# Kernel optimization log

Measured on AMD Instinct MI355X. Metric: run time of the kernel, lower is better.

## Reference

```python
import jax, jax.numpy as jnp
import numpy as np


def _min_euclid_block(x, sh):
    # x: [B, C, T], sh: [C, K, S]
    S = sh.shape[-1]
    T = x.shape[2]
    W = T - S + 1  # number of sliding windows
    idx = jnp.arange(W)[:, None] + jnp.arange(S)[None, :]  # [W, S]
    xu = x[:, :, idx]  # [B, C, W, S] sliding windows (unfold)
    # pairwise euclidean distance via the Gram expansion (same math as cdist)
    x2 = jnp.sum(xu * xu, axis=-1)          # [B, C, W]
    s2 = jnp.sum(sh * sh, axis=-1)          # [C, K]
    xs = jnp.einsum('bcws,cks->bcwk', xu, sh)  # [B, C, W, K]
    d2 = x2[..., None] + s2[None, :, None, :] - 2.0 * xs
    d = jnp.sqrt(jnp.maximum(d2, 1e-12))    # [B, C, W, K]
    d = jnp.sum(d, axis=1, keepdims=True)   # sum over channels -> [B, 1, W, K]
    return jnp.min(d, axis=2)               # min over windows -> [B, 1, K]


def setup_inputs() -> dict:
    key = jax.random.key(0)
    k0, k1, k2, k3 = jax.random.split(key, 4)
    B, C, T, K = 32, 3, 2048, 128
    return {
        'x': jax.random.normal(k0, (B, C, T), dtype=jnp.float32),
        'sh16': jax.random.normal(k1, (C, K, 16), dtype=jnp.float32),
        'sh32': jax.random.normal(k2, (C, K, 32), dtype=jnp.float32),
        'sh64': jax.random.normal(k3, (C, K, 64), dtype=jnp.float32),
    }


def reference(x, sh16, sh32, sh64):
    # ShapeletsDistBlocks with dist_measure='euclidean': run each
    # MinEuclideanDistBlock and concatenate along the shapelet axis (dim 2).
    outs = [_min_euclid_block(x, sh) for sh in (sh16, sh32, sh64)]
    return jnp.concatenate(outs, axis=2)  # [B, 1, sum(K)]
```

## Files before the change

### kernel.cpp

```cpp
#include <hip/hip_runtime.h>

typedef __attribute__((ext_vector_type(8)))  __bf16 bf16x8;
typedef __attribute__((ext_vector_type(16))) float  f32x16;

#define DEV __device__ __forceinline__

namespace {

constexpr int BB = 32, CC = 3, TT = 2048, KK = 128, OUTK = 384;
constexpr int TP = 2176;

constexpr size_t OFF_B16 = 0;
constexpr size_t OFF_B32 = 12288;
constexpr size_t OFF_B64 = 36864;
constexpr size_t OFF_S2  = 86016;
constexpr size_t OFF_X2  = 90624;
constexpr size_t OFF_XC  = 2449920;

DEV unsigned short rne(float f) {
  unsigned u = __float_as_uint(f);
  u += 0x7FFFu + ((u >> 16) & 1u);
  return (unsigned short)(u >> 16);
}
DEV float rnef(float f) {
  unsigned u = __float_as_uint(f);
  u += 0x7FFFu + ((u >> 16) & 1u);
  return __uint_as_float(u & 0xFFFF0000u);
}
DEV uint4 pack8(const unsigned short* h) {
  uint4 d;
  d.x = (unsigned)h[0] | ((unsigned)h[1] << 16);
  d.y = (unsigned)h[2] | ((unsigned)h[3] << 16);
  d.z = (unsigned)h[4] | ((unsigned)h[5] << 16);
  d.w = (unsigned)h[6] | ((unsigned)h[7] << 16);
  return d;
}
DEV float f4get(const float4 v, int j) {
  switch (j) { case 0: return v.x; case 1: return v.y; case 2: return v.z; default: return v.w; }
}

constexpr int N_OUT = BB * OUTK;
constexpr int N_BF  = 5376;
constexpr int N_S2  = 1152;
constexpr int N_XC  = BB * CC * 8 * (TP/8);
constexpr int N_X2  = BB * CC * TT;
constexpr int N_TOT = N_OUT + N_BF + N_S2 + N_XC + N_X2;

__global__ __launch_bounds__(256) void precompute(
    const float* __restrict__ x, const float* __restrict__ sh16,
    const float* __restrict__ sh32, const float* __restrict__ sh64,
    unsigned char* __restrict__ ws, unsigned* __restrict__ outu)
{
  int i = blockIdx.x * 256 + threadIdx.x;
  if (i >= N_TOT) return;
  if (i < N_OUT) { outu[i] = 0x7f800000u; return; }
  i -= N_OUT;

  if (i < N_BF) {
    int S, it; const float* sh; size_t boff;
    if (i < 768)       { S = 16; it = i;        sh = sh16; boff = OFF_B16; }
    else if (i < 2304) { S = 32; it = i - 768;  sh = sh32; boff = OFF_B32; }
    else               { S = 64; it = i - 2304; sh = sh64; boff = OFF_B64; }
    const int CHS = S / 8, KST = S / 16;
    int c = it / (KK * CHS); int r = it - c * KK * CHS;
    int n = r / CHS;         int k0 = (r - n * CHS) * 8;
    const float* src = sh + ((size_t)(c * KK + n)) * S + k0;
    unsigned short h[8];
    #pragma unroll
    for (int j = 0; j < 8; ++j) h[j] = rne(src[j]);
    ((uint4*)(ws + boff))[((c * 4 + (n >> 5)) * KST + (k0 >> 4)) * 64 + ((k0 >> 3) & 1) * 32 + (n & 31)] = pack8(h);
    return;
  }
  i -= N_BF;

  if (i < N_S2) {
    int Sidx = i / 384; int r = i - Sidx * 384; int c = r >> 7; int k = r & 127;
    int S = 16 << Sidx;
    const float* sh = (Sidx == 0) ? sh16 : ((Sidx == 1) ? sh32 : sh64);
    const float* sp = sh + ((size_t)(c * KK + k)) * S;
    float acc = 0.f;
    #pragma unroll 4
    for (int s = 0; s < S; ++s) { float v = rnef(sp[s]); acc = fmaf(v, v, acc); }
    ((float*)(ws + OFF_S2))[(Sidx * CC + c) * KK + k] = acc;
    return;
  }
  i -= N_S2;

  if (i < N_XC) {
    const int per = TP / 8;
    int c8 = i / per; int q8 = i - c8 * per;
    int p  = c8 & 7;  int bc = c8 >> 3;
    const float* xb = x + (size_t)bc * TT;
    int m0 = q8 * 8;
    unsigned short h[8];
    #pragma unroll
    for (int j = 0; j < 8; ++j) {
      int mi = m0 + j + p;
      float v = (mi < TT) ? xb[mi] : 0.f;
      h[j] = rne(v);
    }
    ((uint4*)(ws + OFF_XC + (size_t)c8 * TP * 2))[q8] = pack8(h);
    return;
  }
  i -= N_XC;

  {
    int w = i & (TT - 1); int bc = i >> 11;
    const float* xb = x + (size_t)bc * TT;
    float acc = 0.f, a16, a32, a64;
    #pragma unroll 4
    for (int s = 0; s < 16; ++s) { int mi = w + s; float v = (mi < TT) ? rnef(xb[mi]) : 0.f; acc = fmaf(v, v, acc); }
    a16 = acc;
    #pragma unroll 4
    for (int s = 16; s < 32; ++s) { int mi = w + s; float v = (mi < TT) ? rnef(xb[mi]) : 0.f; acc = fmaf(v, v, acc); }
    a32 = acc;
    #pragma unroll 4
    for (int s = 32; s < 64; ++s) { int mi = w + s; float v = (mi < TT) ? rnef(xb[mi]) : 0.f; acc = fmaf(v, v, acc); }
    a64 = acc;
    float* x2 = (float*)(ws + OFF_X2);
    x2[(size_t)(0 * BB * CC + bc) * TT + w] = a16;
    x2[(size_t)(1 * BB * CC + bc) * TT + w] = a32;
    x2[(size_t)(2 * BB * CC + bc) * TT + w] = a64;
  }
}

DEV void epi(const f32x16 a, const float* __restrict__ x2c, float s2c, int lhi, f32x16& dsum) {
  #pragma unroll
  for (int g = 0; g < 4; ++g) {
    const float4 xq = *(const float4*)(x2c + 4 * lhi + 8 * g);
    #pragma unroll
    for (int j = 0; j < 4; ++j) {
      const int r2 = g * 4 + j;
      dsum[r2] += __builtin_amdgcn_sqrtf(fmaxf(fmaf(-2.f, a[r2], f4get(xq, j) + s2c), 1e-12f));
    }
  }
}

template<int S, int KST, int OUTOFF, size_t BOFF, int SIDX>
DEV void run(const unsigned char* __restrict__ ws, unsigned* __restrict__ outu,
             int r, float* __restrict__ x2l, float* __restrict__ s2l)
{
  const int b = r >> 4, wg = r & 15;
  const int tid = (int)threadIdx.x;
  const int lane = tid & 63, wsub = tid >> 6;
  const int l31 = lane & 31, lhi = lane >> 5, p = l31 & 7;
  const int w0 = wg * 128 + wsub * 32;

  const unsigned short* XCb = (const unsigned short*)(ws + OFF_XC);
  uint4 A[CC][KST];
  #pragma unroll
  for (int c = 0; c < CC; ++c) {
    const unsigned short* xA = XCb + ((size_t)((b * CC + c) * 8) + p) * TP
                             + (w0 + 8 * (l31 >> 3) + 8 * lhi);
    #pragma unroll
    for (int kk = 0; kk < KST; ++kk) A[c][kk] = *(const uint4*)(xA + 16 * kk);
  }

  const float* x2g = (const float*)(ws + OFF_X2) + (size_t)(SIDX * BB * CC + b * CC) * TT + wg * 128;
  const float* s2g = (const float*)(ws + OFF_S2) + SIDX * CC * KK;
  #pragma unroll
  for (int i0 = 0; i0 < 2; ++i0) {
    int i = i0 * 256 + tid;
    if (i < 384) {
      int c = i >> 7, q = i & 127;
      x2l[i] = x2g[(size_t)c * TT + q];
      s2l[i] = s2g[c * KK + q];
    }
  }
  __syncthreads();

  const uint4* Bg = (const uint4*)(ws + BOFF) + lane;
  constexpr int W = TT - S + 1;

  #pragma unroll
  for (int kq = 0; kq < 4; ++kq) {
    f32x16 dsum{};
    #pragma unroll
    for (int c = 0; c < CC; ++c) {
      uint4 Bf[KST];
      #pragma unroll
      for (int kk = 0; kk < KST; ++kk)
        Bf[kk] = Bg[(size_t)(((c * 4 + kq) * KST + kk)) * 64];
      f32x16 acc{};
      #pragma unroll
      for (int kk = 0; kk < KST; ++kk)
        acc = __builtin_amdgcn_mfma_f32_32x32x16_bf16(
            __builtin_bit_cast(bf16x8, A[c][kk]), __builtin_bit_cast(bf16x8, Bf[kk]), acc, 0, 0, 0);
      const float s2c = s2l[c * 128 + kq * 32 + l31];
      epi(acc, x2l + c * 128 + wsub * 32, s2c, lhi, dsum);
    }
    float m = __builtin_inff();
    if (w0 + 31 < W) {
      #pragma unroll
      for (int r2 = 0; r2 < 16; ++r2) m = fminf(m, dsum[r2]);
    } else {
      #pragma unroll
      for (int r2 = 0; r2 < 16; ++r2) {
        const int ro = (r2 & 3) + 8 * (r2 >> 2) + 4 * lhi;
        if (w0 + ro < W) m = fminf(m, dsum[r2]);
      }
    }
    m = fminf(m, __shfl_xor(m, 32));
    if (lane < 32)
      atomicMin(outu + (b * OUTK + OUTOFF + kq * 32 + l31), __float_as_uint(m));
  }
}

__global__ __launch_bounds__(256, 3) void shapelets_main(
    const unsigned char* __restrict__ ws, unsigned* __restrict__ outu)
{
  __shared__ __attribute__((aligned(16))) float x2l[384];
  __shared__ __attribute__((aligned(16))) float s2l[384];
  const int j = (int)blockIdx.x;
  if (j < 512)       run<64, 4, 256, OFF_B64, 2>(ws, outu, j,        x2l, s2l);
  else if (j < 1024) run<32, 2, 128, OFF_B32, 1>(ws, outu, j - 512,  x2l, s2l);
  else               run<16, 1,   0, OFF_B16, 0>(ws, outu, j - 1024, x2l, s2l);
}

}

extern "C" void kernel_launch(void* const* d_in, const int* in_sizes, int n_in,
                              void* d_out, int out_size, void* d_ws, size_t ws_size,
                              hipStream_t stream) {
  const float* x    = (const float*)d_in[0];
  const float* sh16 = (const float*)d_in[1];
  const float* sh32 = (const float*)d_in[2];
  const float* sh64 = (const float*)d_in[3];
  unsigned* outu = (unsigned*)d_out;
  unsigned char* ws = (unsigned char*)d_ws;

  precompute<<<(N_TOT + 255) / 256, 256, 0, stream>>>(x, sh16, sh32, sh64, ws, outu);
  shapelets_main<<<1536, 256, 0, stream>>>(ws, outu);
}
```

Measured before the change: 39.72 us.

## Stage shapelet B fragments through double-buffered LDS with cooperative prefetch

Each block previously had all four waves load the same shapelet B fragments from global memory. The block now loads them cooperatively into a double-buffered LDS staging area, prefetching the next kq chunk into registers while the current one is computed, with a barrier per chunk. The atomicMin writes are also deferred to the end of the block. This cuts redundant global/L2 traffic, but it adds about 24KB of LDS per block, four barriers, and staging registers, which may lower occupancy.

New measurement: 42.69 us. 7.5% more time.

```diff
diff --git a/kernel.cpp b/kernel.cpp
--- a/kernel.cpp
+++ b/kernel.cpp
@@ -136,10 +136,37 @@
   }
 }
 
+template<int KST>
+DEV void stageLoad(const uint4* __restrict__ Bg0, int kq, int tid, uint4 (&st)[3]) {
+  constexpr int TOT = CC * KST * 64;
+  constexpr int NJ  = (TOT + 255) / 256;
+  #pragma unroll
+  for (int j = 0; j < NJ; ++j) {
+    int i = j * 256 + tid;
+    if ((TOT % 256 == 0) || i < TOT) {
+      int slot = i & 63, m = i >> 6;
+      int c = m / KST, kk = m - c * KST;
+      st[j] = Bg0[(size_t)(((c * 4 + kq) * KST + kk)) * 64 + slot];
+    }
+  }
+}
+template<int KST>
+DEV void stageWrite(uint4* __restrict__ lbuf, int tid, const uint4 (&st)[3]) {
+  constexpr int TOT = CC * KST * 64;
+  constexpr int NJ  = (TOT + 255) / 256;
+  #pragma unroll
+  for (int j = 0; j < NJ; ++j) {
+    int i = j * 256 + tid;
+    if ((TOT % 256 == 0) || i < TOT) lbuf[i] = st[j];
+  }
+}
+
 template<int S, int KST, int OUTOFF, size_t BOFF, int SIDX>
 DEV void run(const unsigned char* __restrict__ ws, unsigned* __restrict__ outu,
-             int r, float* __restrict__ x2l, float* __restrict__ s2l)
+             int r, float* __restrict__ x2l, float* __restrict__ s2l,
+             uint4* __restrict__ bbuf)
 {
+  constexpr int CHUNK = CC * KST * 64;
   const int b = r >> 4, wg = r & 15;
   const int tid = (int)threadIdx.x;
   const int lane = tid & 63, wsub = tid >> 6;
@@ -155,6 +182,10 @@
     #pragma unroll
     for (int kk = 0; kk < KST; ++kk) A[c][kk] = *(const uint4*)(xA + 16 * kk);
   }
+
+  const uint4* Bg0 = (const uint4*)(ws + BOFF);
+  uint4 st[3];
+  stageLoad<KST>(Bg0, 0, tid, st);
 
   const float* x2g = (const float*)(ws + OFF_X2) + (size_t)(SIDX * BB * CC + b * CC) * TT + wg * 128;
   const float* s2g = (const float*)(ws + OFF_S2) + SIDX * CC * KK;
@@ -167,20 +198,23 @@
       s2l[i] = s2g[c * KK + q];
     }
   }
+  stageWrite<KST>(bbuf, tid, st);
   __syncthreads();
 
-  const uint4* Bg = (const uint4*)(ws + BOFF) + lane;
   constexpr int W = TT - S + 1;
+  float mq[4];
 
   #pragma unroll
   for (int kq = 0; kq < 4; ++kq) {
+    if (kq < 3) stageLoad<KST>(Bg0, kq + 1, tid, st);
+    const uint4* lb = bbuf + (kq & 1) * CHUNK;
     f32x16 dsum{};
     #pragma unroll
     for (int c = 0; c < CC; ++c) {
       uint4 Bf[KST];
       #pragma unroll
       for (int kk = 0; kk < KST; ++kk)
-        Bf[kk] = Bg[(size_t)(((c * 4 + kq) * KST + kk)) * 64];
+        Bf[kk] = lb[(c * KST + kk) * 64 + lane];
       f32x16 acc{};
       #pragma unroll
       for (int kk = 0; kk < KST; ++kk)
@@ -200,9 +234,17 @@
         if (w0 + ro < W) m = fminf(m, dsum[r2]);
       }
     }
-    m = fminf(m, __shfl_xor(m, 32));
-    if (lane < 32)
-      atomicMin(outu + (b * OUTK + OUTOFF + kq * 32 + l31), __float_as_uint(m));
+    mq[kq] = fminf(m, __shfl_xor(m, 32));
+    if (kq < 3) {
+      stageWrite<KST>(bbuf + ((kq & 1) ^ 1) * CHUNK, tid, st);
+      __syncthreads();
+    }
+  }
+
+  if (lane < 32) {
+    #pragma unroll
+    for (int kq = 0; kq < 4; ++kq)
+      atomicMin(outu + (b * OUTK + OUTOFF + kq * 32 + l31), __float_as_uint(mq[kq]));
   }
 }
 
@@ -211,10 +253,11 @@
 {
   __shared__ __attribute__((aligned(16))) float x2l[384];
   __shared__ __attribute__((aligned(16))) float s2l[384];
+  __shared__ __attribute__((aligned(16))) uint4 bbuf[2 * CC * 4 * 64];
   const int j = (int)blockIdx.x;
-  if (j < 512)       run<64, 4, 256, OFF_B64, 2>(ws, outu, j,        x2l, s2l);
-  else if (j < 1024) run<32, 2, 128, OFF_B32, 1>(ws, outu, j - 512,  x2l, s2l);
-  else               run<16, 1,   0, OFF_B16, 0>(ws, outu, j - 1024, x2l, s2l);
+  if (j < 512)       run<64, 4, 256, OFF_B64, 2>(ws, outu, j,        x2l, s2l, bbuf);
+  else if (j < 1024) run<32, 2, 128, OFF_B32, 1>(ws, outu, j - 512,  x2l, s2l, bbuf);
+  else               run<16, 1,   0, OFF_B16, 0>(ws, outu, j - 1024, x2l, s2l, bbuf);
 }
 
 }
```

## Use single-wave blocks and read x2/s2 from global instead of LDS

Applied to the files above, without the earlier changes.

The main kernel now runs one 64-thread wavefront per block (6144 blocks) instead of four wavefronts per 256-thread block. Each wave reads its x2 and s2 values directly from global memory (relying on cache) rather than staging them in shared memory behind a __syncthreads. This removes the LDS staging step and the block barrier and gives finer scheduling granularity. In exchange there are more block launches and more global/L1 traffic for the epilogue operands.

New measurement: 49.82 us. 25.4% more time.

```diff
diff --git a/kernel.cpp b/kernel.cpp
--- a/kernel.cpp
+++ b/kernel.cpp
@@ -137,14 +137,12 @@
 }
 
 template<int S, int KST, int OUTOFF, size_t BOFF, int SIDX>
-DEV void run(const unsigned char* __restrict__ ws, unsigned* __restrict__ outu,
-             int r, float* __restrict__ x2l, float* __restrict__ s2l)
+DEV void run(const unsigned char* __restrict__ ws, unsigned* __restrict__ outu, int widx)
 {
-  const int b = r >> 4, wg = r & 15;
-  const int tid = (int)threadIdx.x;
-  const int lane = tid & 63, wsub = tid >> 6;
+  const int b = widx >> 6, t = widx & 63;
+  const int lane = (int)threadIdx.x & 63;
   const int l31 = lane & 31, lhi = lane >> 5, p = l31 & 7;
-  const int w0 = wg * 128 + wsub * 32;
+  const int w0 = t * 32;
 
   const unsigned short* XCb = (const unsigned short*)(ws + OFF_XC);
   uint4 A[CC][KST];
@@ -156,19 +154,8 @@
     for (int kk = 0; kk < KST; ++kk) A[c][kk] = *(const uint4*)(xA + 16 * kk);
   }
 
-  const float* x2g = (const float*)(ws + OFF_X2) + (size_t)(SIDX * BB * CC + b * CC) * TT + wg * 128;
+  const float* x2g = (const float*)(ws + OFF_X2) + (size_t)(SIDX * BB * CC + b * CC) * TT + w0;
   const float* s2g = (const float*)(ws + OFF_S2) + SIDX * CC * KK;
-  #pragma unroll
-  for (int i0 = 0; i0 < 2; ++i0) {
-    int i = i0 * 256 + tid;
-    if (i < 384) {
-      int c = i >> 7, q = i & 127;
-      x2l[i] = x2g[(size_t)c * TT + q];
-      s2l[i] = s2g[c * KK + q];
-    }
-  }
-  __syncthreads();
-
   const uint4* Bg = (const uint4*)(ws + BOFF) + lane;
   constexpr int W = TT - S + 1;
 
@@ -186,8 +173,8 @@
       for (int kk = 0; kk < KST; ++kk)
         acc = __builtin_amdgcn_mfma_f32_32x32x16_bf16(
             __builtin_bit_cast(bf16x8, A[c][kk]), __builtin_bit_cast(bf16x8, Bf[kk]), acc, 0, 0, 0);
-      const float s2c = s2l[c * 128 + kq * 32 + l31];
-      epi(acc, x2l + c * 128 + wsub * 32, s2c, lhi, dsum);
+      const float s2c = s2g[c * KK + kq * 32 + l31];
+      epi(acc, x2g + (size_t)c * TT, s2c, lhi, dsum);
     }
     float m = __builtin_inff();
     if (w0 + 31 < W) {
@@ -206,15 +193,13 @@
   }
 }
 
-__global__ __launch_bounds__(256, 3) void shapelets_main(
+__global__ __launch_bounds__(64, 4) void shapelets_main(
     const unsigned char* __restrict__ ws, unsigned* __restrict__ outu)
 {
-  __shared__ __attribute__((aligned(16))) float x2l[384];
-  __shared__ __attribute__((aligned(16))) float s2l[384];
   const int j = (int)blockIdx.x;
-  if (j < 512)       run<64, 4, 256, OFF_B64, 2>(ws, outu, j,        x2l, s2l);
-  else if (j < 1024) run<32, 2, 128, OFF_B32, 1>(ws, outu, j - 512,  x2l, s2l);
-  else               run<16, 1,   0, OFF_B16, 0>(ws, outu, j - 1024, x2l, s2l);
+  if (j < 2048)      run<64, 4, 256, OFF_B64, 2>(ws, outu, j);
+  else if (j < 4096) run<32, 2, 128, OFF_B32, 1>(ws, outu, j - 2048);
+  else               run<16, 1,   0, OFF_B16, 0>(ws, outu, j - 4096);
 }
 
 }
@@ -230,5 +215,5 @@
   unsigned char* ws = (unsigned char*)d_ws;
 
   precompute<<<(N_TOT + 255) / 256, 256, 0, stream>>>(x, sh16, sh32, sh64, ws, outu);
-  shapelets_main<<<1536, 256, 0, stream>>>(ws, outu);
-}
+  shapelets_main<<<6144, 64, 0, stream>>>(ws, outu);
+}
```

## Stage shapelet B fragments in LDS and process two window groups per block

Applied to the files above, without the earlier changes.

Each block now loads the whole bf16 shapelet fragment set for its scale into shared memory once, instead of every wave reading it from global memory inside the kq loop. Each block also handles two window groups (h=0,1), which halves the grid from 1536 to 768 blocks and spreads the B staging cost over twice as much work. The price is extra LDS (up to 48KB of B fragments plus a larger x2 buffer), which may lower occupancy below the 3 blocks/CU target. It also serialises the two window groups inside each block.

After: 69.94 us. 76.1% more time.

```diff
diff --git a/kernel.cpp b/kernel.cpp
--- a/kernel.cpp
+++ b/kernel.cpp
@@ -138,83 +138,101 @@
 
 template<int S, int KST, int OUTOFF, size_t BOFF, int SIDX>
 DEV void run(const unsigned char* __restrict__ ws, unsigned* __restrict__ outu,
-             int r, float* __restrict__ x2l, float* __restrict__ s2l)
+             int r, float* __restrict__ x2l, float* __restrict__ s2l,
+             uint4* __restrict__ bbuf)
 {
-  const int b = r >> 4, wg = r & 15;
+  constexpr int BTOT = CC * 4 * KST * 64;
+  constexpr int NJ   = BTOT / 256;
+  const int b = r >> 3, wgp = r & 7;
   const int tid = (int)threadIdx.x;
   const int lane = tid & 63, wsub = tid >> 6;
   const int l31 = lane & 31, lhi = lane >> 5, p = l31 & 7;
-  const int w0 = wg * 128 + wsub * 32;
-
-  const unsigned short* XCb = (const unsigned short*)(ws + OFF_XC);
-  uint4 A[CC][KST];
-  #pragma unroll
-  for (int c = 0; c < CC; ++c) {
-    const unsigned short* xA = XCb + ((size_t)((b * CC + c) * 8) + p) * TP
-                             + (w0 + 8 * (l31 >> 3) + 8 * lhi);
-    #pragma unroll
-    for (int kk = 0; kk < KST; ++kk) A[c][kk] = *(const uint4*)(xA + 16 * kk);
-  }
-
-  const float* x2g = (const float*)(ws + OFF_X2) + (size_t)(SIDX * BB * CC + b * CC) * TT + wg * 128;
+
+  const uint4* Bg0 = (const uint4*)(ws + BOFF);
+  uint4 st[NJ];
+  #pragma unroll
+  for (int j = 0; j < NJ; ++j) st[j] = Bg0[j * 256 + tid];
+
+  const float* x2g = (const float*)(ws + OFF_X2) + (size_t)(SIDX * BB * CC + b * CC) * TT;
   const float* s2g = (const float*)(ws + OFF_S2) + SIDX * CC * KK;
+  #pragma unroll
+  for (int i0 = 0; i0 < 3; ++i0) {
+    int i = i0 * 256 + tid;
+    int h = i / 384, q = i % 384;
+    int c = q >> 7, w = q & 127;
+    x2l[i] = x2g[(size_t)c * TT + (wgp + h * 8) * 128 + w];
+  }
   #pragma unroll
   for (int i0 = 0; i0 < 2; ++i0) {
     int i = i0 * 256 + tid;
-    if (i < 384) {
-      int c = i >> 7, q = i & 127;
-      x2l[i] = x2g[(size_t)c * TT + q];
-      s2l[i] = s2g[c * KK + q];
-    }
-  }
+    if (i < 384) s2l[i] = s2g[i];
+  }
+  #pragma unroll
+  for (int j = 0; j < NJ; ++j) bbuf[j * 256 + tid] = st[j];
   __syncthreads();
 
-  const uint4* Bg = (const uint4*)(ws + BOFF) + lane;
+  const unsigned short* XCb = (const unsigned short*)(ws + OFF_XC);
   constexpr int W = TT - S + 1;
 
-  #pragma unroll
-  for (int kq = 0; kq < 4; ++kq) {
-    f32x16 dsum{};
+  #pragma unroll 1
+  for (int h = 0; h < 2; ++h) {
+    const int wg = wgp + h * 8;
+    const int w0 = wg * 128 + wsub * 32;
+
+    uint4 A[CC][KST];
     #pragma unroll
     for (int c = 0; c < CC; ++c) {
-      uint4 Bf[KST];
+      const unsigned short* xA = XCb + ((size_t)((b * CC + c) * 8) + p) * TP
+                               + (w0 + 8 * (l31 >> 3) + 8 * lhi);
       #pragma unroll
-      for (int kk = 0; kk < KST; ++kk)
-        Bf[kk] = Bg[(size_t)(((c * 4 + kq) * KST + kk)) * 64];
-      f32x16 acc{};
+      for (int kk = 0; kk < KST; ++kk) A[c][kk] = *(const uint4*)(xA + 16 * kk);
+    }
+
+    #pragma unroll
+    for (int kq = 0; kq < 4; ++kq) {
+      f32x16 dsum{};
       #pragma unroll
-      for (int kk = 0; kk < KST; ++kk)
-        acc = __builtin_amdgcn_mfma_f32_32x32x16_bf16(
-            __builtin_bit_cast(bf16x8, A[c][kk]), __builtin_bit_cast(bf16x8, Bf[kk]), acc, 0, 0, 0);
-      const float s2c = s2l[c * 128 + kq * 32 + l31];
-      epi(acc, x2l + c * 128 + wsub * 32, s2c, lhi, dsum);
-    }
-    float m = __builtin_inff();
-    if (w0 + 31 < W) {
-      #pragma unroll
-      for (int r2 = 0; r2 < 16; ++r2) m = fminf(m, dsum[r2]);
-    } else {
-      #pragma unroll
-      for (int r2 = 0; r2 < 16; ++r2) {
-        const int ro = (r2 & 3) + 8 * (r2 >> 2) + 4 * lhi;
-        if (w0 + ro < W) m = fminf(m, dsum[r2]);
+      for (int c = 0; c < CC; ++c) {
+        uint4 Bf[KST];
+        #pragma unroll
+        for (int kk = 0; kk < KST; ++kk)
+          Bf[kk] = bbuf[((c * 4 + kq) * KST + kk) * 64 + lane];
+        f32x16 acc{};
+        #pragma unroll
+        for (int kk = 0; kk < KST; ++kk)
+          acc = __builtin_amdgcn_mfma_f32_32x32x16_bf16(
+              __builtin_bit_cast(bf16x8, A[c][kk]), __builtin_bit_cast(bf16x8, Bf[kk]), acc, 0, 0, 0);
+        const float s2c = s2l[c * 128 + kq * 32 + l31];
+        epi(acc, x2l + h * 384 + c * 128 + wsub * 32, s2c, lhi, dsum);
       }
-    }
-    m = fminf(m, __shfl_xor(m, 32));
-    if (lane < 32)
-      atomicMin(outu + (b * OUTK + OUTOFF + kq * 32 + l31), __float_as_uint(m));
+      float m = __builtin_inff();
+      if (w0 + 31 < W) {
+        #pragma unroll
+        for (int r2 = 0; r2 < 16; ++r2) m = fminf(m, dsum[r2]);
+      } else {
+        #pragma unroll
+        for (int r2 = 0; r2 < 16; ++r2) {
+          const int ro = (r2 & 3) + 8 * (r2 >> 2) + 4 * lhi;
+          if (w0 + ro < W) m = fminf(m, dsum[r2]);
+        }
+      }
+      m = fminf(m, __shfl_xor(m, 32));
+      if (lane < 32)
+        atomicMin(outu + (b * OUTK + OUTOFF + kq * 32 + l31), __float_as_uint(m));
+    }
   }
 }
 
 __global__ __launch_bounds__(256, 3) void shapelets_main(
     const unsigned char* __restrict__ ws, unsigned* __restrict__ outu)
 {
-  __shared__ __attribute__((aligned(16))) float x2l[384];
+  __shared__ __attribute__((aligned(16))) float x2l[768];
   __shared__ __attribute__((aligned(16))) float s2l[384];
+  __shared__ __attribute__((aligned(16))) uint4 bbuf[CC * 4 * 4 * 64];
   const int j = (int)blockIdx.x;
-  if (j < 512)       run<64, 4, 256, OFF_B64, 2>(ws, outu, j,        x2l, s2l);
-  else if (j < 1024) run<32, 2, 128, OFF_B32, 1>(ws, outu, j - 512,  x2l, s2l);
-  else               run<16, 1,   0, OFF_B16, 0>(ws, outu, j - 1024, x2l, s2l);
+  if (j < 256)      run<64, 4, 256, OFF_B64, 2>(ws, outu, j,       x2l, s2l, bbuf);
+  else if (j < 512) run<32, 2, 128, OFF_B32, 1>(ws, outu, j - 256, x2l, s2l, bbuf);
+  else              run<16, 1,   0, OFF_B16, 0>(ws, outu, j - 512, x2l, s2l, bbuf);
 }
 
 }
@@ -230,5 +248,5 @@
   unsigned char* ws = (unsigned char*)d_ws;
 
   precompute<<<(N_TOT + 255) / 256, 256, 0, stream>>>(x, sh16, sh32, sh64, ws, outu);
-  shapelets_main<<<1536, 256, 0, stream>>>(ws, outu);
-}
+  shapelets_main<<<768, 256, 0, stream>>>(ws, outu);
+}
```
